# Kernel optimization log

Measured on AMD Instinct MI355X. Metric: run time of the kernel, lower is better.

The kernel has to match this reference:

```python
import jax, jax.numpy as jnp
import numpy as np

N_HEADS = 16
D_HEAD = 64
CHUNK = 64


@jax.custom_vjp
def binarize(x):
    return jnp.where(x >= 0, 1.0, -1.0).astype(x.dtype)

def _bin_fwd(x):
    return binarize(x), x

def _bin_bwd(x, g):
    return (g * (jnp.abs(x) <= 1.0).astype(g.dtype),)

binarize.defvjp(_bin_fwd, _bin_bwd)


def setup_inputs() -> dict:
    key = jax.random.key(0)
    k1, k2, k3 = jax.random.split(key, 3)
    B, T, D = 4, 4096, 1024
    x = jax.random.normal(k1, (B, T, D), dtype=jnp.float32)
    W_qkv = jax.random.normal(k2, (3 * D, D), dtype=jnp.float32) * 0.02
    W_o = jax.random.normal(k3, (D, D), dtype=jnp.float32) * 0.02
    return {"x": x, "W_qkv": W_qkv, "W_o": W_o}


def reference(x, W_qkv, W_o):
    B, T, D = x.shape
    H, d, C = N_HEADS, D_HEAD, CHUNK
    scale = 1.0 / (d ** 0.5)

    qkv = (x @ W_qkv.T).reshape(B, T, 3, H, d)
    q = jnp.swapaxes(qkv[:, :, 0], 1, 2) * scale   # [B,H,T,d]
    k = binarize(jnp.swapaxes(qkv[:, :, 1], 1, 2))
    v = binarize(jnp.swapaxes(qkv[:, :, 2], 1, 2))

    N = T // C  # T chosen divisible by chunk size (pad branch is a no-op)
    qc = q.reshape(B, H, N, C, d)
    kc = k.reshape(B, H, N, C, d)
    vc = v.reshape(B, H, N, C, d)

    mask = jnp.tril(jnp.ones((C, C), dtype=x.dtype))
    intra_scores = jnp.einsum('bhnid,bhnjd->bhnij', qc, kc) * mask
    intra = jnp.einsum('bhnij,bhnjd->bhnid', intra_scores, vc)

    chunk_kv = jnp.einsum('bhnck,bhncd->bhnkd', kc, vc)          # [B,H,N,d,d]
    ckv32 = chunk_kv.astype(jnp.float32)
    prefix = (jnp.cumsum(ckv32, axis=2) - ckv32).astype(chunk_kv.dtype)
    cross = jnp.einsum('bhnck,bhnkd->bhncd', qc, prefix)

    pos = jnp.arange(1, C + 1, dtype=x.dtype)
    offs = jnp.arange(N, dtype=x.dtype) * C
    total = jnp.clip(offs[:, None] + pos[None, :], 1.0, None).reshape(1, 1, N, C, 1)

    out = ((intra + cross) / total).reshape(B, H, T, d)
    out = jnp.swapaxes(out, 1, 2).reshape(B, T, D)
    y = out @ W_o.T

    final_matrix = prefix[:, :, -1] + chunk_kv[:, :, -1]          # [B,H,d,d]
    final_count = jnp.full((B, H, 1, 1), T, dtype=x.dtype)
    return (y, final_matrix, final_count)
```

## Files before the change

### kernel.cpp

```cpp
#include <hip/hip_runtime.h>
#include <cstdint>

#define B_ 4
#define T_ 4096
#define D_ 1024
#define H_ 16
#define HD_ 64
#define N_ 64

typedef __attribute__((ext_vector_type(8))) short s16x8;
typedef __attribute__((ext_vector_type(4))) float f32x4;

__device__ __forceinline__ unsigned short f2bf(float f) {
    unsigned int u = __builtin_bit_cast(unsigned int, f);
    u += 0x7fffu + ((u >> 16) & 1u);
    return (unsigned short)(u >> 16);
}
__device__ __forceinline__ float bf2f(unsigned short h) {
    unsigned int u = ((unsigned int)h) << 16;
    return __builtin_bit_cast(float, u);
}
__device__ __forceinline__ void gl2lds(const short* g, short* l) {
    __builtin_amdgcn_global_load_lds(
        (const __attribute__((address_space(1))) void*)g,
        (__attribute__((address_space(3))) void*)l, 16, 0, 0);
}
#define MFMA16(a, b, c) __builtin_amdgcn_mfma_f32_16x16x32_bf16(a, b, c, 0, 0, 0)
#define SB0() __builtin_amdgcn_sched_barrier(0)
#define BAR() __builtin_amdgcn_s_barrier()

#define BF_P1 ((short)0x3F80)
#define BF_M1 ((short)0xBF80)

__global__ __launch_bounds__(256)
void k_cvt(const float* __restrict__ in, short* __restrict__ out, int n4)
{
    int i = blockIdx.x * blockDim.x + threadIdx.x;
    const int stride = gridDim.x * blockDim.x;
    for (; i < n4; i += stride) {
        float4 f = ((const float4*)in)[i];
        short4 o;
        o.x = (short)f2bf(f.x); o.y = (short)f2bf(f.y);
        o.z = (short)f2bf(f.z); o.w = (short)f2bf(f.w);
        *(short4*)(out + i * 4) = o;
    }
}

template<int MODE, int KD, int NCB>
__global__ __launch_bounds__(256, 2)
void k_gemm3(const short* __restrict__ A, const short* __restrict__ Bm,
             short* __restrict__ Oq, signed char* __restrict__ K8,
             signed char* __restrict__ V8, float* __restrict__ Yf)
{
    __shared__ __align__(16) short LS[2][2][8192];

    const int tid = threadIdx.x;
    const int nwg = 128 * NCB;
    const int bid = blockIdx.x;
    const int sz  = (bid & 7) * (nwg >> 3) + (bid >> 3);
    const int cb  = sz % NCB, rb = sz / NCB;
    const int row0 = rb * 128, col0 = cb * 128;

    const int lane = tid & 63, w = tid >> 6;
    const int wr = w >> 1, wc = w & 1;
    const int cl = lane & 15, rg = lane >> 4;

    const int sr8 = lane >> 3;
    const int slg = ((lane & 7) ^ sr8) * 8;
    const short* gA = A  + (size_t)(row0 + w * 32 + sr8) * KD + slg;
    const short* gB = Bm + (size_t)(col0 + w * 32 + sr8) * KD + slg;

    f32x4 acc[4][4];
    #pragma unroll
    for (int i = 0; i < 4; ++i)
        #pragma unroll
        for (int j = 0; j < 4; ++j) acc[i][j] = (f32x4)0.f;

    auto stage = [&](int pb, int t) {
        const int ko = t * 64;
        #pragma unroll
        for (int c = 0; c < 4; ++c) {
            gl2lds(gA + ko + (size_t)c * 8 * KD, &LS[pb][0][(w * 32 + c * 8) * 64]);
            gl2lds(gB + ko + (size_t)c * 8 * KD, &LS[pb][1][(w * 32 + c * 8) * 64]);
        }
    };
    auto ldf = [&](const short* base, int R, int q) -> s16x8 {
        return *(const s16x8*)((const char*)base + R * 128 + ((q ^ (R & 7)) << 4));
    };

    const int nt = KD / 64;
    stage(0, 0);
    for (int t = 0; t < nt; ++t) {
        const int pb = t & 1;
        if (t + 1 < nt) {
            stage(pb ^ 1, t + 1);
            asm volatile("s_waitcnt vmcnt(8)" ::: "memory");
        } else {
            asm volatile("s_waitcnt vmcnt(0)" ::: "memory");
        }
        BAR();
        SB0();
        const short* bA = &LS[pb][0][0];
        const short* bB = &LS[pb][1][0];
        #pragma unroll
        for (int kk = 0; kk < 2; ++kk) {
            s16x8 fb[4];
            #pragma unroll
            for (int ni = 0; ni < 4; ++ni)
                fb[ni] = ldf(bB, wc * 64 + ni * 16 + cl, kk * 4 + rg);
            #pragma unroll
            for (int mi = 0; mi < 4; ++mi) {
                s16x8 fa = ldf(bA, wr * 64 + mi * 16 + cl, kk * 4 + rg);
                __builtin_amdgcn_s_setprio(1);
                #pragma unroll
                for (int ni = 0; ni < 4; ++ni)
                    acc[mi][ni] = MFMA16(fa, fb[ni], acc[mi][ni]);
                __builtin_amdgcn_s_setprio(0);
            }
        }
        SB0();
        BAR();
    }

    const int m0 = row0 + wr * 64, n0 = col0 + wc * 64;
    if (MODE == 0) {
        const int s = col0 >> 10;
        #pragma unroll
        for (int ni = 0; ni < 4; ++ni) {
            const int col = n0 + ni * 16 + cl;
            const int h = (col & 1023) >> 6, dd = col & 63;
            #pragma unroll
            for (int mi = 0; mi < 4; ++mi)
                #pragma unroll
                for (int r = 0; r < 4; ++r) {
                    const int bt = m0 + mi * 16 + rg * 4 + r;
                    const int bb = bt >> 12, t = bt & (T_ - 1);
                    const size_t bh64 = (size_t)(bb * H_ + h);
                    const float v = acc[mi][ni][r];
                    if (s == 0) {
                        Oq[(bh64 * T_ + t) * 64 + dd] =
                            (short)f2bf(v * 0.125f);
                    } else if (s == 1) {
                        K8[(bh64 * T_ + t) * 64 + dd] =
                            (v >= 0.f) ? 1 : -1;
                    } else {
                        const size_t otr = bh64 * ((size_t)T_ * 64)
                                         + (size_t)(t >> 6) * 4096 + dd * 64 + (t & 63);
                        V8[otr] = (v >= 0.f) ? 1 : -1;
                    }
                }
        }
    } else {
        #pragma unroll
        for (int ni = 0; ni < 4; ++ni) {
            const int col = n0 + ni * 16 + cl;
            #pragma unroll
            for (int mi = 0; mi < 4; ++mi)
                #pragma unroll
                for (int r = 0; r < 4; ++r)
                    Yf[(size_t)(m0 + mi * 16 + rg * 4 + r) * D_ + col] =
                        acc[mi][ni][r];
        }
    }
}

template<int MODE, int KD, int NCB>
__global__ __launch_bounds__(512, 4)
void k_gemm2(const short* __restrict__ A, const short* __restrict__ Bm,
             short* __restrict__ Oq, signed char* __restrict__ K8,
             signed char* __restrict__ V8, float* __restrict__ Yf)
{
    __shared__ __align__(16) short LA[256 * 64];
    __shared__ __align__(16) short LB[128 * 64];

    const int tid = threadIdx.x;
    const int nwg = 64 * NCB;
    const int bid = blockIdx.x;
    const int sz  = (bid & 7) * (nwg >> 3) + (bid >> 3);
    const int cb  = sz % NCB, rb = sz / NCB;
    const int row0 = rb * 256, col0 = cb * 128;

    const int lane = tid & 63, w = tid >> 6;
    const int wr = w >> 1, wc = w & 1;
    const int cl = lane & 15, rg = lane >> 4;

    const int sr8 = lane >> 3;
    const int slg = ((lane & 7) ^ sr8) * 8;
    const short* gA = A  + (size_t)(row0 + w * 32 + sr8) * KD + slg;
    const short* gB = Bm + (size_t)(col0 + w * 16 + sr8) * KD + slg;

    f32x4 acc[4][4];
    #pragma unroll
    for (int i = 0; i < 4; ++i)
        #pragma unroll
        for (int j = 0; j < 4; ++j) acc[i][j] = (f32x4)0.f;

    auto stage = [&](int t) {
        const int ko = t * 64;
        #pragma unroll
        for (int c = 0; c < 4; ++c)
            gl2lds(gA + ko + (size_t)c * 8 * KD, &LA[(w * 32 + c * 8) * 64]);
        #pragma unroll
        for (int c = 0; c < 2; ++c)
            gl2lds(gB + ko + (size_t)c * 8 * KD, &LB[(w * 16 + c * 8) * 64]);
    };
    auto ldf = [&](const short* base, int R, int q) -> s16x8 {
        return *(const s16x8*)((const char*)base + R * 128 + ((q ^ (R & 7)) << 4));
    };

    const int nt = KD / 64;
    stage(0);
    for (int t = 0; t < nt; ++t) {
        asm volatile("s_waitcnt vmcnt(0)" ::: "memory");
        BAR();
        SB0();
        #pragma unroll
        for (int kk = 0; kk < 2; ++kk) {
            s16x8 fb[4];
            #pragma unroll
            for (int ni = 0; ni < 4; ++ni)
                fb[ni] = ldf(LB, wc * 64 + ni * 16 + cl, kk * 4 + rg);
            #pragma unroll
            for (int mi = 0; mi < 4; ++mi) {
                s16x8 fa = ldf(LA, wr * 64 + mi * 16 + cl, kk * 4 + rg);
                __builtin_amdgcn_s_setprio(1);
                #pragma unroll
                for (int ni = 0; ni < 4; ++ni)
                    acc[mi][ni] = MFMA16(fa, fb[ni], acc[mi][ni]);
                __builtin_amdgcn_s_setprio(0);
            }
        }
        SB0();
        BAR();
        if (t + 1 < nt) stage(t + 1);
    }

    const int m0 = row0 + wr * 64, n0 = col0 + wc * 64;
    if (MODE == 1) {
        #pragma unroll
        for (int ni = 0; ni < 4; ++ni) {
            const int col = n0 + ni * 16 + cl;
            #pragma unroll
            for (int mi = 0; mi < 4; ++mi)
                #pragma unroll
                for (int r = 0; r < 4; ++r)
                    Yf[(size_t)(m0 + mi * 16 + rg * 4 + r) * D_ + col] =
                        acc[mi][ni][r];
        }
    }
}

__global__ __launch_bounds__(256)
void k_chunkA(const signed char* __restrict__ Kb8,
              const signed char* __restrict__ VbT8,
              signed char* __restrict__ CKV8)
{
    __shared__ __align__(16) short KTs[4096], VTs[4096];
    __shared__ __align__(16) signed char Cs8[4096];
    const int tid = threadIdx.x;
    const int bh = blockIdx.x >> 6, n = blockIdx.x & 63;
    const size_t kbase = ((size_t)bh * T_ + n * 64) * 64;
    const size_t vbase = (size_t)bh * T_ * 64 + (size_t)n * 4096;

    {
        const int off = tid * 16;
        int4 vr = *(const int4*)(VbT8 + vbase + off);
        const signed char* vb = (const signed char*)&vr;
        const int vrow = off >> 6, vcb = off & 63;
        #pragma unroll
        for (int jj = 0; jj < 2; ++jj) {
            s16x8 v;
            #pragma unroll
            for (int j = 0; j < 8; ++j)
                v[j] = (vb[jj*8+j] >= 0) ? BF_P1 : BF_M1;
            const int o = (vrow * 128 + (vcb + jj * 8) * 2) ^ ((vrow & 7) << 4);
            *(s16x8*)((char*)VTs + o) = v;
        }
        int4 kr = *(const int4*)(Kb8 + kbase + off);
        const signed char* kb = (const signed char*)&kr;
        const int c = off >> 6, d0 = off & 63;
        #pragma unroll
        for (int j = 0; j < 16; ++j) {
            const int dd = d0 + j;
            const short sv = (kb[j] >= 0) ? BF_P1 : BF_M1;
            const int o2 = (dd * 128 + c * 2) ^ ((dd & 7) << 4);
            *(short*)((char*)KTs + o2) = sv;
        }
    }
    __syncthreads();

    const int lane = tid & 63, w = tid >> 6;
    const int cl = lane & 15, rg = lane >> 4;
    auto frag = [&](const short* l, int rowbase, int kk) -> s16x8 {
        const int row = rowbase + cl;
        int off = row * 128 + kk * 64 + rg * 16;
        off ^= (row & 7) << 4;
        return *(const s16x8*)((const char*)l + off);
    };

    f32x4 a3[4];
    #pragma unroll
    for (int ni = 0; ni < 4; ++ni) a3[ni] = (f32x4)0.f;
    const s16x8 va0 = frag(VTs, w * 16, 0), va1 = frag(VTs, w * 16, 1);
    #pragma unroll
    for (int ni = 0; ni < 4; ++ni) {
        a3[ni] = MFMA16(va0, frag(KTs, ni * 16, 0), a3[ni]);
        a3[ni] = MFMA16(va1, frag(KTs, ni * 16, 1), a3[ni]);
    }
    #pragma unroll
    for (int ni = 0; ni < 4; ++ni)
        #pragma unroll
        for (int r = 0; r < 4; ++r) {
            const int m = w * 16 + rg * 4 + r;
            const int c = ni * 16 + cl;
            Cs8[m * 64 + c] = (signed char)(int)a3[ni][r];
        }
    __syncthreads();
    const size_t c8 = ((size_t)bh * 64 + n) * 4096;
    *(int4*)(CKV8 + c8 + tid * 16) = *(const int4*)(Cs8 + tid * 16);
}

__global__ __launch_bounds__(256)
void k_scan2(const signed char* __restrict__ CKV8, short* __restrict__ PB,
             float* __restrict__ FM, float* __restrict__ FC)
{
    const int bh = blockIdx.x >> 4;
    const int e  = (blockIdx.x & 15) * 256 + threadIdx.x;
    const size_t b8 = (size_t)bh * N_ * 4096 + e;
    const size_t bp = (size_t)bh * N_ * 4096 + e;
    int run = 0;
    #pragma unroll
    for (int nn = 0; nn < 64; ++nn) {
        PB[bp + (size_t)nn * 4096] = (short)f2bf((float)run);
        run += (int)CKV8[b8 + (size_t)nn * 4096];
    }
    FM[(size_t)bh * 4096 + (e & 63) * 64 + (e >> 6)] = (float)run;
    if ((blockIdx.x & 15) == 0 && threadIdx.x == 0) FC[bh] = (float)T_;
}

__global__ __launch_bounds__(256)
void k_cross3(const short* __restrict__ Qb, const signed char* __restrict__ Kb8,
              const signed char* __restrict__ VbT8, const short* __restrict__ PB,
              short* __restrict__ OMb)
{
    __shared__ __align__(16) short Qs[4096], Ks[4096], VTs[4096], Ps[4096], Ss[4096];
    const int tid = threadIdx.x;
    const int bh = blockIdx.x >> 6, n = blockIdx.x & 63;
    const size_t cbase = ((size_t)bh * T_ + n * 64) * 64;
    const size_t kbase = cbase;
    const size_t vbase = (size_t)bh * T_ * 64 + (size_t)n * 4096;

    auto stage_tile = [&](const short* g, short* l) {
        #pragma unroll
        for (int p = 0; p < 2; ++p) {
            const int off = tid * 16 + p * 4096;
            const int r = off >> 7;
            s16x8 v = *(const s16x8*)(g + (off >> 1));
            *(s16x8*)((char*)l + (off ^ ((r & 7) << 4))) = v;
        }
    };
    stage_tile(Qb + cbase, Qs);
    stage_tile(PB + ((size_t)bh * 64 + n) * 4096, Ps);
    {
        const int off = tid * 16;
        int4 kr = *(const int4*)(Kb8 + kbase + off);
        const signed char* kb = (const signed char*)&kr;
        int4 vr = *(const int4*)(VbT8 + vbase + off);
        const signed char* vb = (const signed char*)&vr;
        const int row = off >> 6, cb = off & 63;
        #pragma unroll
        for (int jj = 0; jj < 2; ++jj) {
            s16x8 kv, vv;
            #pragma unroll
            for (int j = 0; j < 8; ++j) {
                kv[j] = (kb[jj*8+j] >= 0) ? BF_P1 : BF_M1;
                vv[j] = (vb[jj*8+j] >= 0) ? BF_P1 : BF_M1;
            }
            const int o = (row * 128 + (cb + jj * 8) * 2) ^ ((row & 7) << 4);
            *(s16x8*)((char*)Ks  + o) = kv;
            *(s16x8*)((char*)VTs + o) = vv;
        }
    }
    __syncthreads();

    const int lane = tid & 63, w = tid >> 6;
    const int cl = lane & 15, rg = lane >> 4;
    auto frag = [&](const short* l, int rowbase, int kk) -> s16x8 {
        const int row = rowbase + cl;
        int off = row * 128 + kk * 64 + rg * 16;
        off ^= (row & 7) << 4;
        return *(const s16x8*)((const char*)l + off);
    };

    const s16x8 qa0 = frag(Qs, w * 16, 0), qa1 = frag(Qs, w * 16, 1);
    {
        f32x4 a1[4];
        #pragma unroll
        for (int ni = 0; ni < 4; ++ni) a1[ni] = (f32x4)0.f;
        #pragma unroll
        for (int ni = 0; ni < 4; ++ni) {
            a1[ni] = MFMA16(qa0, frag(Ks, ni * 16, 0), a1[ni]);
            a1[ni] = MFMA16(qa1, frag(Ks, ni * 16, 1), a1[ni]);
        }
        #pragma unroll
        for (int ni = 0; ni < 4; ++ni)
            #pragma unroll
            for (int r = 0; r < 4; ++r) {
                const int i = w * 16 + rg * 4 + r, j = ni * 16 + cl;
                const float v = (j <= i) ? a1[ni][r] : 0.f;
                const int off = (i * 128 + j * 2) ^ ((i & 7) << 4);
                *(short*)((char*)Ss + off) = (short)f2bf(v);
            }
    }
    __syncthreads();

    {
        f32x4 a2[4], a3[4];
        #pragma unroll
        for (int ni = 0; ni < 4; ++ni) { a2[ni] = (f32x4)0.f; a3[ni] = (f32x4)0.f; }
        const s16x8 sa0 = frag(Ss, w * 16, 0), sa1 = frag(Ss, w * 16, 1);
        #pragma unroll
        for (int ni = 0; ni < 4; ++ni) {
            a2[ni] = MFMA16(sa0, frag(VTs, ni * 16, 0), a2[ni]);
            a2[ni] = MFMA16(sa1, frag(VTs, ni * 16, 1), a2[ni]);
            a3[ni] = MFMA16(qa0, frag(Ps, ni * 16, 0), a3[ni]);
            a3[ni] = MFMA16(qa1, frag(Ps, ni * 16, 1), a3[ni]);
        }
        #pragma unroll
        for (int ni = 0; ni < 4; ++ni)
            #pragma unroll
            for (int r = 0; r < 4; ++r) {
                const int i = w * 16 + rg * 4 + r, j = ni * 16 + cl;
                const float invt = 1.0f / (float)(n * 64 + i + 1);
                const float f = (a2[ni][r] + a3[ni][r]) * invt;
                const int off = (i * 128 + j * 2) ^ ((i & 7) << 4);
                *(short*)((char*)Qs + off) = (short)f2bf(f);
            }
    }
    __syncthreads();

    const int bb = bh >> 4, h = bh & 15;
    #pragma unroll
    for (int p = 0; p < 2; ++p) {
        const int off = tid * 16 + p * 4096;
        const int r = off >> 7;
        const int lo = off ^ ((r & 7) << 4);
        s16x8 v = *(const s16x8*)((char*)Qs + lo);
        const size_t gi = ((size_t)bb * T_ + n * 64 + r) * D_
                        + h * 64 + ((off & 127) >> 1);
        *(s16x8*)(OMb + gi) = v;
    }
}

extern "C" void kernel_launch(void* const* d_in, const int* in_sizes, int n_in,
                              void* d_out, int out_size, void* d_ws, size_t ws_size,
                              hipStream_t stream)
{
    const float* X    = (const float*)d_in[0];
    const float* Wqkv = (const float*)d_in[1];
    const float* Wo   = (const float*)d_in[2];

    float* Y  = (float*)d_out;
    float* FM = Y + (size_t)B_ * T_ * D_;
    float* FC = FM + (size_t)B_ * H_ * HD_ * HD_;

    char* ws = (char*)d_ws;
    const size_t Mi = 1048576;
    short*       Qb     = (short*)(ws + 0 * Mi);
    signed char* Kb8    = (signed char*)(ws + 32 * Mi);
    signed char* VbT8   = (signed char*)(ws + 48 * Mi);
    short*       PB     = (short*)(ws + 64 * Mi);
    short*       Xb     = (short*)(ws + 96 * Mi);
    short*       OMb    = (short*)(ws + 96 * Mi);
    signed char* CKV8   = (signed char*)(ws + 128 * Mi);
    short*       Wqkvb  = (short*)(ws + 144 * Mi);
    short*       WoS    = (short*)(ws + 150 * Mi);
    if (ws_size < (size_t)152 * Mi) return;

    dim3 blk(256), blkg(512);
    k_cvt<<<dim3(2048), blk, 0, stream>>>(X, Xb, 4194304);
    k_cvt<<<dim3(1024), blk, 0, stream>>>(Wqkv, Wqkvb, 786432);
    k_gemm3<0, 1024, 24><<<dim3(3072), blk, 0, stream>>>(Xb, Wqkvb, Qb, Kb8, VbT8, nullptr);
    k_chunkA<<<dim3(4096), blk, 0, stream>>>(Kb8, VbT8, CKV8);
    k_scan2 <<<dim3(1024), blk, 0, stream>>>(CKV8, PB, FM, FC);
    k_cross3<<<dim3(4096), blk, 0, stream>>>(Qb, Kb8, VbT8, PB, OMb);
    k_cvt<<<dim3(512), blk, 0, stream>>>(Wo, WoS, 262144);
    k_gemm2<1, 1024, 8><<<dim3(512), blkg, 0, stream>>>(OMb, WoS, nullptr, nullptr, nullptr, Y);
}
```

Before: 272.5 us.

## Merge fp32-to-bf16 conversions into one launch and halve QKV GEMM K-tile

The three fp32-to-bf16 conversion kernels (x, W_qkv, W_o) are merged into a single launch, saving two kernel launches. The QKV projection GEMM now stages a K-depth of 32 per step instead of 64. That halves its LDS footprint and lets launch bounds request four workgroups per CU instead of two. The new swizzle and staging pattern, with fewer loads per stage, trades double the barrier count per K for higher occupancy and better latency hiding.

After: 278.4 us. +2.2%, slower.

```diff
diff --git a/kernel.cpp b/kernel.cpp
--- a/kernel.cpp
+++ b/kernel.cpp
@@ -33,26 +33,35 @@
 #define BF_M1 ((short)0xBF80)
 
 __global__ __launch_bounds__(256)
-void k_cvt(const float* __restrict__ in, short* __restrict__ out, int n4)
-{
+void k_cvt3(const float* __restrict__ inX,  short* __restrict__ outX,  int nX,
+            const float* __restrict__ inW,  short* __restrict__ outW,  int nW,
+            const float* __restrict__ inO,  short* __restrict__ outO,  int nO)
+{
+    const int ntot = nX + nW + nO;
     int i = blockIdx.x * blockDim.x + threadIdx.x;
     const int stride = gridDim.x * blockDim.x;
-    for (; i < n4; i += stride) {
-        float4 f = ((const float4*)in)[i];
+    for (; i < ntot; i += stride) {
+        const float* src;
+        short* dst;
+        int j = i;
+        if (j < nX)            { src = inX; dst = outX; }
+        else if (j < nX + nW)  { j -= nX; src = inW; dst = outW; }
+        else                   { j -= nX + nW; src = inO; dst = outO; }
+        float4 f = ((const float4*)src)[j];
         short4 o;
         o.x = (short)f2bf(f.x); o.y = (short)f2bf(f.y);
         o.z = (short)f2bf(f.z); o.w = (short)f2bf(f.w);
-        *(short4*)(out + i * 4) = o;
+        *(short4*)(dst + j * 4) = o;
     }
 }
 
 template<int MODE, int KD, int NCB>
-__global__ __launch_bounds__(256, 2)
-void k_gemm3(const short* __restrict__ A, const short* __restrict__ Bm,
+__global__ __launch_bounds__(256, 4)
+void k_gemm6(const short* __restrict__ A, const short* __restrict__ Bm,
              short* __restrict__ Oq, signed char* __restrict__ K8,
              signed char* __restrict__ V8, float* __restrict__ Yf)
 {
-    __shared__ __align__(16) short LS[2][2][8192];
+    __shared__ __align__(16) short LS[2][2][4096];
 
     const int tid = threadIdx.x;
     const int nwg = 128 * NCB;
@@ -65,10 +74,10 @@
     const int wr = w >> 1, wc = w & 1;
     const int cl = lane & 15, rg = lane >> 4;
 
-    const int sr8 = lane >> 3;
-    const int slg = ((lane & 7) ^ sr8) * 8;
-    const short* gA = A  + (size_t)(row0 + w * 32 + sr8) * KD + slg;
-    const short* gB = Bm + (size_t)(col0 + w * 32 + sr8) * KD + slg;
+    const int sr  = lane >> 2;
+    const int ssl = ((lane & 3) - ((lane >> 3) & 3)) & 3;
+    const short* gA = A  + (size_t)(row0 + w * 32 + sr) * KD + ssl * 8;
+    const short* gB = Bm + (size_t)(col0 + w * 32 + sr) * KD + ssl * 8;
 
     f32x4 acc[4][4];
     #pragma unroll
@@ -77,24 +86,24 @@
         for (int j = 0; j < 4; ++j) acc[i][j] = (f32x4)0.f;
 
     auto stage = [&](int pb, int t) {
-        const int ko = t * 64;
-        #pragma unroll
-        for (int c = 0; c < 4; ++c) {
-            gl2lds(gA + ko + (size_t)c * 8 * KD, &LS[pb][0][(w * 32 + c * 8) * 64]);
-            gl2lds(gB + ko + (size_t)c * 8 * KD, &LS[pb][1][(w * 32 + c * 8) * 64]);
-        }
+        const int ko = t * 32;
+        gl2lds(gA + ko,                   &LS[pb][0][(w * 32     ) * 32]);
+        gl2lds(gA + ko + (size_t)16 * KD, &LS[pb][0][(w * 32 + 16) * 32]);
+        gl2lds(gB + ko,                   &LS[pb][1][(w * 32     ) * 32]);
+        gl2lds(gB + ko + (size_t)16 * KD, &LS[pb][1][(w * 32 + 16) * 32]);
     };
     auto ldf = [&](const short* base, int R, int q) -> s16x8 {
-        return *(const s16x8*)((const char*)base + R * 128 + ((q ^ (R & 7)) << 4));
-    };
-
-    const int nt = KD / 64;
+        const int off = R * 64 + (((q + (R >> 1)) & 3) << 4);
+        return *(const s16x8*)((const char*)base + off);
+    };
+
+    const int nt = KD / 32;
     stage(0, 0);
     for (int t = 0; t < nt; ++t) {
         const int pb = t & 1;
         if (t + 1 < nt) {
             stage(pb ^ 1, t + 1);
-            asm volatile("s_waitcnt vmcnt(8)" ::: "memory");
+            asm volatile("s_waitcnt vmcnt(4)" ::: "memory");
         } else {
             asm volatile("s_waitcnt vmcnt(0)" ::: "memory");
         }
@@ -102,21 +111,18 @@
         SB0();
         const short* bA = &LS[pb][0][0];
         const short* bB = &LS[pb][1][0];
-        #pragma unroll
-        for (int kk = 0; kk < 2; ++kk) {
-            s16x8 fb[4];
+        s16x8 fb[4];
+        #pragma unroll
+        for (int ni = 0; ni < 4; ++ni)
+            fb[ni] = ldf(bB, wc * 64 + ni * 16 + cl, rg);
+        #pragma unroll
+        for (int mi = 0; mi < 4; ++mi) {
+            s16x8 fa = ldf(bA, wr * 64 + mi * 16 + cl, rg);
+            __builtin_amdgcn_s_setprio(1);
             #pragma unroll
             for (int ni = 0; ni < 4; ++ni)
-                fb[ni] = ldf(bB, wc * 64 + ni * 16 + cl, kk * 4 + rg);
-            #pragma unroll
-            for (int mi = 0; mi < 4; ++mi) {
-                s16x8 fa = ldf(bA, wr * 64 + mi * 16 + cl, kk * 4 + rg);
-                __builtin_amdgcn_s_setprio(1);
-                #pragma unroll
-                for (int ni = 0; ni < 4; ++ni)
-                    acc[mi][ni] = MFMA16(fa, fb[ni], acc[mi][ni]);
-                __builtin_amdgcn_s_setprio(0);
-            }
+                acc[mi][ni] = MFMA16(fa, fb[ni], acc[mi][ni]);
+            __builtin_amdgcn_s_setprio(0);
         }
         SB0();
         BAR();
@@ -478,12 +484,12 @@
     if (ws_size < (size_t)152 * Mi) return;
 
     dim3 blk(256), blkg(512);
-    k_cvt<<<dim3(2048), blk, 0, stream>>>(X, Xb, 4194304);
-    k_cvt<<<dim3(1024), blk, 0, stream>>>(Wqkv, Wqkvb, 786432);
-    k_gemm3<0, 1024, 24><<<dim3(3072), blk, 0, stream>>>(Xb, Wqkvb, Qb, Kb8, VbT8, nullptr);
+    k_cvt3<<<dim3(2048), blk, 0, stream>>>(X, Xb, 4194304,
+                                           Wqkv, Wqkvb, 786432,
+                                           Wo, WoS, 262144);
+    k_gemm6<0, 1024, 24><<<dim3(3072), blk, 0, stream>>>(Xb, Wqkvb, Qb, Kb8, VbT8, nullptr);
     k_chunkA<<<dim3(4096), blk, 0, stream>>>(Kb8, VbT8, CKV8);
     k_scan2 <<<dim3(1024), blk, 0, stream>>>(CKV8, PB, FM, FC);
     k_cross3<<<dim3(4096), blk, 0, stream>>>(Qb, Kb8, VbT8, PB, OMb);
-    k_cvt<<<dim3(512), blk, 0, stream>>>(Wo, WoS, 262144);
     k_gemm2<1, 1024, 8><<<dim3(512), blkg, 0, stream>>>(OMb, WoS, nullptr, nullptr, nullptr, Y);
 }
```
